# Optimization experiments

Hardware: AMD Instinct MI355X
Metric: run time of the kernel (lower is better)

Reference implementation:

```python
import jax, jax.numpy as jnp
import numpy as np

N, C, L, D, F = 8, 128, 512, 64, 512
ATTN_W = 64
LN_EPS = 1e-5
ATTN_EPS = 1e-6


def _xavier(k, shape):
    lim = float(np.sqrt(6.0 / (shape[0] + shape[1])))
    return jax.random.uniform(k, shape, jnp.float32, -lim, lim)


def setup_inputs() -> dict:
    key = jax.random.key(0)
    ks = jax.random.split(key, 8)
    return dict(
        x=jax.random.normal(ks[0], (N, C, L), jnp.float32),
        Wx=_xavier(ks[1], (C, D)),
        Wt=_xavier(ks[2], (C, D)),
        bh=jnp.zeros((D,), jnp.float32),
        Wa=_xavier(ks[3], (D, 1)),
        ba=jnp.zeros((1,), jnp.float32),
        W0=_xavier(ks[4], (C, F)),
        b0=jnp.zeros((F,), jnp.float32),
        W1=_xavier(ks[5], (F, C)),
        b1=jnp.zeros((C,), jnp.float32),
        g0=jnp.ones((C,), jnp.float32),
        be0=jnp.zeros((C,), jnp.float32),
        g1=jnp.ones((C,), jnp.float32),
        be1=jnp.zeros((C,), jnp.float32),
    )


def _layernorm(y, g, b):
    mu = jnp.mean(y, axis=-1, keepdims=True)
    var = jnp.var(y, axis=-1, keepdims=True)
    return (y - mu) * jax.lax.rsqrt(var + LN_EPS) * g + b


def reference(x, Wx, Wt, bh, Wa, ba, W0, b0, W1, b1, g0, be0, g1, be1):
    xt = jnp.transpose(x, (0, 2, 1))  # (N, L, C)
    q = jnp.einsum('nlc,cd->nld', xt, Wt)  # (N, L, D)
    k = jnp.einsum('nlc,cd->nld', xt, Wx)  # (N, L, D)
    # additive (Bahdanau) scores: h is the large (N, L, L, D) intermediate
    h = jnp.tanh(q[:, :, None, :] + k[:, None, :, :] + bh)
    e = jnp.einsum('nlmd,d->nlm', h, Wa[:, 0]) + ba[0]  # (N, L, L)
    e = jnp.exp(e - jnp.max(e, axis=-1, keepdims=True))
    # local band mask: tril(w//2 - 1) & triu(-w//2) on (row i, col j)
    dij = jnp.arange(L)[None, :] - jnp.arange(L)[:, None]  # j - i
    mask = (dij <= ATTN_W // 2 - 1) & (dij >= -(ATTN_W // 2))
    e = jnp.where(mask, e, 0.0)
    a = e / (jnp.sum(e, axis=-1, keepdims=True) + ATTN_EPS)  # (N, L, L)
    v = jnp.einsum('nlm,nmc->nlc', a, xt)  # (N, L, C)
    x2 = _layernorm(v + xt, g0, be0)
    x3 = jnp.einsum('nlf,fc->nlc', jax.nn.relu(jnp.einsum('nlc,cf->nlf', x2, W0) + b0), W1) + b1
    x4 = _layernorm(x3 + x2, g1, be1)
    return (jnp.transpose(x4, (0, 2, 1)), a)
```

## Files before the change

kernel.cpp:

```cpp
#include <hip/hip_runtime.h>
#include <cstddef>


__global__ __launch_bounds__(256) void prep_kernel(
    const float* __restrict__ x, const float* __restrict__ Wt,
    const float* __restrict__ Wx, float* __restrict__ xt,
    float* __restrict__ q, float* __restrict__ k) {
  __shared__ float xs[128][17];
  int tid = threadIdx.x;
  int bz = blockIdx.x;
  int n = bz >> 6;
  int t6 = bz & 63;
  int l0 = (t6 >> 1) << 4;
  int which = t6 & 1;

  for (int idx = tid; idx < 512; idx += 256) {
    int c = idx >> 2, v = idx & 3;
    float4 d4 = *(const float4*)(x + ((size_t)n * 128 + c) * 512 + l0 + 4 * v);
    xs[c][4 * v + 0] = d4.x; xs[c][4 * v + 1] = d4.y;
    xs[c][4 * v + 2] = d4.z; xs[c][4 * v + 3] = d4.w;
  }
  __syncthreads();

  if (which == 0) {
    for (int idx = tid; idx < 2048; idx += 256) {
      int c = idx & 127, jj = idx >> 7;
      xt[((size_t)n * 512 + l0 + jj) * 128 + c] = xs[c][jj];
    }
  }

  const float* W = which ? Wx : Wt;
  float* dst = which ? k : q;
  int r = tid >> 4;
  int f0 = (tid & 15) << 2;
  float acc[4] = {0.f, 0.f, 0.f, 0.f};
#pragma unroll 4
  for (int cc = 0; cc < 128; cc++) {
    float xv = xs[cc][r];
    float4 w = *(const float4*)(W + cc * 64 + f0);
    acc[0] += xv * w.x; acc[1] += xv * w.y;
    acc[2] += xv * w.z; acc[3] += xv * w.w;
  }
  *(float4*)(dst + ((size_t)n * 512 + l0 + r) * 64 + f0) =
      make_float4(acc[0], acc[1], acc[2], acc[3]);
}

__global__ __launch_bounds__(512, 2) void attn_ffn_fused_kernel(
    const float* __restrict__ q, const float* __restrict__ k,
    const float* __restrict__ bh, const float* __restrict__ Wa,
    const float* __restrict__ ba, const float* __restrict__ xt,
    const float* __restrict__ g0, const float* __restrict__ be0,
    const float* __restrict__ W0, const float* __restrict__ b0,
    const float* __restrict__ W1, const float* __restrict__ b1,
    const float* __restrict__ g1, const float* __restrict__ be1,
    float* __restrict__ a, float* __restrict__ out) {
  __shared__ __align__(16) char smem[81920];
  __shared__ float xst[128][20];
  __shared__ float av[16][64];
  __shared__ float was[64];

  float (*ks)[65] = (float(*)[65])smem;
  float (*qs)[64] = (float(*)[64])(smem + 20544);
  float (*tst)[20] = (float(*)[20])smem;
  float (*part)[16][128] = (float(*)[16][128])(smem + 40960);
  float (*ys)[128] = (float(*)[128])(smem + 73728);

  int tid = threadIdx.x;
  int w = tid >> 6, lane = tid & 63;
  size_t rbase = (size_t)blockIdx.x * 16;
  int n = (int)(rbase >> 9);
  int i0 = (int)(rbase & 511);
  int jlo0 = i0 - 32;

  if (tid < 64) was[tid] = Wa[tid];
  for (int idx = tid; idx < 16 * 16; idx += 512) {
    int r = idx >> 4, d4 = (idx & 15) << 2;
    float4 qv = *(const float4*)(q + ((size_t)n * 512 + i0 + r) * 64 + d4);
    float4 bv = *(const float4*)(bh + d4);
    *(float4*)(&qs[r][d4]) =
        make_float4(qv.x + bv.x, qv.y + bv.y, qv.z + bv.z, qv.w + bv.w);
  }
  for (int idx = tid; idx < 79 * 16; idx += 512) {
    int row = idx >> 4, d4 = (idx & 15) << 2;
    int j = jlo0 + row;
    float4 v = make_float4(0.f, 0.f, 0.f, 0.f);
    if (j >= 0 && j < 512)
      v = *(const float4*)(k + ((size_t)n * 512 + j) * 64 + d4);
    ks[row][d4 + 0] = v.x; ks[row][d4 + 1] = v.y;
    ks[row][d4 + 2] = v.z; ks[row][d4 + 3] = v.w;
  }
  __syncthreads();

#pragma unroll
  for (int rr = 0; rr < 2; rr++) {
    int r = 2 * w + rr;
    int i = i0 + r;
    int j = jlo0 + r + lane;
    bool valid = (j >= 0 && j < 512);
    const float* krow = &ks[r + lane][0];
    float e = 0.f;
#pragma unroll 8
    for (int d = 0; d < 64; d++) {
      float hx = qs[r][d] + krow[d];
      float ex2 = __expf(2.f * hx);
      float th = 1.f - 2.f * __builtin_amdgcn_rcpf(ex2 + 1.f);
      e += was[d] * th;
    }
    e += ba[0];
    if (!valid) e = -1e30f;

    float m = e;
    for (int o = 32; o > 0; o >>= 1) m = fmaxf(m, __shfl_xor(m, o, 64));
    float ex = valid ? __expf(e - m) : 0.f;
    float s = ex;
    for (int o = 32; o > 0; o >>= 1) s += __shfl_xor(s, o, 64);
    av[r][lane] = ex / (s + 1e-6f);

    float* arow = a + ((size_t)n * 512 + i) * 512;
    int jlo = i - 32;
#pragma unroll
    for (int t = 0; t < 2; t++) {
      int col0 = 4 * lane + 256 * t;
      float4 v;
      { int jr = col0 + 0 - jlo; int jc = min(max(jr, 0), 63); v.x = (jr >= 0 && jr < 64) ? av[r][jc] : 0.f; }
      { int jr = col0 + 1 - jlo; int jc = min(max(jr, 0), 63); v.y = (jr >= 0 && jr < 64) ? av[r][jc] : 0.f; }
      { int jr = col0 + 2 - jlo; int jc = min(max(jr, 0), 63); v.z = (jr >= 0 && jr < 64) ? av[r][jc] : 0.f; }
      { int jr = col0 + 3 - jlo; int jc = min(max(jr, 0), 63); v.w = (jr >= 0 && jr < 64) ? av[r][jc] : 0.f; }
      *(float4*)(arow + col0) = v;
    }
  }
  __syncthreads();

  {
    int c = tid & 127;
    int rq = tid >> 7;
    int r0 = rq << 2;
    const float* xtn = xt + (size_t)n * 512 * 128;
    float acc[4] = {0.f, 0.f, 0.f, 0.f};
    int jlo = i0 + r0 - 32;
#pragma unroll
    for (int mm = 0; mm < 67; mm++) {
      int jj = jlo + mm;
      int jc = min(max(jj, 0), 511);
      float xv = xtn[(size_t)jc * 128 + c];
#pragma unroll
      for (int rr = 0; rr < 4; rr++) {
        int mr = mm - rr;
        if (mr >= 0 && mr < 64) acc[rr] += av[r0 + rr][mr] * xv;
      }
    }
#pragma unroll
    for (int rr = 0; rr < 4; rr++) {
      float res = xtn[(size_t)(i0 + r0 + rr) * 128 + c];
      xst[c][r0 + rr] = acc[rr] + res;
    }
  }
  __syncthreads();

#pragma unroll
  for (int rr = 2 * w; rr <= 2 * w + 1; rr++) {
    float a0 = xst[lane][rr], a1 = xst[lane + 64][rr];
    float s = a0 + a1, s2 = a0 * a0 + a1 * a1;
    for (int o = 32; o > 0; o >>= 1) {
      s += __shfl_xor(s, o, 64);
      s2 += __shfl_xor(s2, o, 64);
    }
    float mu = s * (1.f / 128.f);
    float var = s2 * (1.f / 128.f) - mu * mu;
    float rs = rsqrtf(var + 1e-5f);
    xst[lane][rr] = (a0 - mu) * rs * g0[lane] + be0[lane];
    xst[lane + 64][rr] = (a1 - mu) * rs * g0[lane + 64] + be0[lane + 64];
  }
  __syncthreads();

  {
    int fb = tid & 127;
    int r0 = (tid >> 7) << 2;
    float acc[4][4];
#pragma unroll
    for (int i = 0; i < 4; i++)
#pragma unroll
      for (int jj = 0; jj < 4; jj++) acc[i][jj] = 0.f;
#pragma unroll 4
    for (int cc = 0; cc < 128; cc++) {
      float4 xv = *(const float4*)(&xst[cc][r0]);
      float w0 = W0[cc * 512 + fb];
      float w1 = W0[cc * 512 + fb + 128];
      float w2 = W0[cc * 512 + fb + 256];
      float w3 = W0[cc * 512 + fb + 384];
      acc[0][0] += xv.x * w0; acc[1][0] += xv.y * w0; acc[2][0] += xv.z * w0; acc[3][0] += xv.w * w0;
      acc[0][1] += xv.x * w1; acc[1][1] += xv.y * w1; acc[2][1] += xv.z * w1; acc[3][1] += xv.w * w1;
      acc[0][2] += xv.x * w2; acc[1][2] += xv.y * w2; acc[2][2] += xv.z * w2; acc[3][2] += xv.w * w2;
      acc[0][3] += xv.x * w3; acc[1][3] += xv.y * w3; acc[2][3] += xv.z * w3; acc[3][3] += xv.w * w3;
    }
#pragma unroll
    for (int jj = 0; jj < 4; jj++) {
      int f = fb + 128 * jj;
      float bb = b0[f];
      float4 v = make_float4(fmaxf(acc[0][jj] + bb, 0.f), fmaxf(acc[1][jj] + bb, 0.f),
                             fmaxf(acc[2][jj] + bb, 0.f), fmaxf(acc[3][jj] + bb, 0.f));
      *(float4*)(&tst[f][r0]) = v;
    }
  }
  __syncthreads();

  {
    int kq = tid >> 7;
    int c0 = (tid & 31) << 2;
    int r0 = ((tid >> 5) & 3) << 2;
    float acc[4][4];
#pragma unroll
    for (int i = 0; i < 4; i++)
#pragma unroll
      for (int jj = 0; jj < 4; jj++) acc[i][jj] = 0.f;
    const float* W1p = W1 + (size_t)kq * 128 * 128;
    const float(*tstp)[20] = &tst[kq * 128];
#pragma unroll 4
    for (int t = 0; t < 128; t++) {
      float4 wv = *(const float4*)(W1p + t * 128 + c0);
      float4 tv = *(const float4*)(&tstp[t][r0]);
      acc[0][0] += tv.x * wv.x; acc[0][1] += tv.x * wv.y; acc[0][2] += tv.x * wv.z; acc[0][3] += tv.x * wv.w;
      acc[1][0] += tv.y * wv.x; acc[1][1] += tv.y * wv.y; acc[1][2] += tv.y * wv.z; acc[1][3] += tv.y * wv.w;
      acc[2][0] += tv.z * wv.x; acc[2][1] += tv.z * wv.y; acc[2][2] += tv.z * wv.z; acc[2][3] += tv.z * wv.w;
      acc[3][0] += tv.w * wv.x; acc[3][1] += tv.w * wv.y; acc[3][2] += tv.w * wv.z; acc[3][3] += tv.w * wv.w;
    }
#pragma unroll
    for (int i = 0; i < 4; i++) {
      *(float4*)(&part[kq][r0 + i][c0]) =
          make_float4(acc[i][0], acc[i][1], acc[i][2], acc[i][3]);
    }
  }
  __syncthreads();

  for (int idx = tid; idx < 2048; idx += 512) {
    int r = idx >> 7, c = idx & 127;
    ys[r][c] = part[0][r][c] + part[1][r][c] + part[2][r][c] + part[3][r][c] +
               b1[c] + xst[c][r];
  }
  __syncthreads();

#pragma unroll
  for (int rr = 2 * w; rr <= 2 * w + 1; rr++) {
    float a0 = ys[rr][lane], a1 = ys[rr][lane + 64];
    float s = a0 + a1, s2 = a0 * a0 + a1 * a1;
    for (int o = 32; o > 0; o >>= 1) {
      s += __shfl_xor(s, o, 64);
      s2 += __shfl_xor(s2, o, 64);
    }
    float mu = s * (1.f / 128.f);
    float var = s2 * (1.f / 128.f) - mu * mu;
    float rs = rsqrtf(var + 1e-5f);
    ys[rr][lane] = (a0 - mu) * rs * g1[lane] + be1[lane];
    ys[rr][lane + 64] = (a1 - mu) * rs * g1[lane + 64] + be1[lane + 64];
  }
  __syncthreads();

  {
    int c = tid >> 2, tq = tid & 3;
    int l0 = (int)(rbase & 511);
    float4 v = make_float4(ys[4 * tq + 0][c], ys[4 * tq + 1][c],
                           ys[4 * tq + 2][c], ys[4 * tq + 3][c]);
    *(float4*)(out + ((size_t)n * 128 + c) * 512 + l0 + 4 * tq) = v;
  }
}

extern "C" void kernel_launch(void* const* d_in, const int* in_sizes, int n_in,
                              void* d_out, int out_size, void* d_ws, size_t ws_size,
                              hipStream_t stream) {
  const float* x   = (const float*)d_in[0];
  const float* Wx  = (const float*)d_in[1];
  const float* Wt  = (const float*)d_in[2];
  const float* bh  = (const float*)d_in[3];
  const float* Wa  = (const float*)d_in[4];
  const float* ba  = (const float*)d_in[5];
  const float* W0  = (const float*)d_in[6];
  const float* b0  = (const float*)d_in[7];
  const float* W1  = (const float*)d_in[8];
  const float* b1  = (const float*)d_in[9];
  const float* g0  = (const float*)d_in[10];
  const float* be0 = (const float*)d_in[11];
  const float* g1  = (const float*)d_in[12];
  const float* be1 = (const float*)d_in[13];

  float* outx = (float*)d_out;
  float* outa = outx + (size_t)524288;

  float* ws = (float*)d_ws;
  float* xt = ws;
  float* q  = xt + 524288;
  float* k  = q + 262144;

  prep_kernel<<<512, 256, 0, stream>>>(x, Wt, Wx, xt, q, k);
  attn_ffn_fused_kernel<<<256, 512, 0, stream>>>(
      q, k, bh, Wa, ba, xt, g0, be0, W0, b0, W1, b1, g1, be1, outa, outx);
}
```

Before: 132.2 us.

## Halve rows per block to double grid and restructure FFN smem layouts

```diff
diff --git a/kernel.cpp b/kernel.cpp
--- a/kernel.cpp
+++ b/kernel.cpp
@@ -45,7 +45,7 @@
       make_float4(acc[0], acc[1], acc[2], acc[3]);
 }
 
-__global__ __launch_bounds__(512, 2) void attn_ffn_fused_kernel(
+__global__ __launch_bounds__(256, 2) void attn_ffn_fused_kernel(
     const float* __restrict__ q, const float* __restrict__ k,
     const float* __restrict__ bh, const float* __restrict__ Wa,
     const float* __restrict__ ba, const float* __restrict__ xt,
@@ -54,33 +54,33 @@
     const float* __restrict__ W1, const float* __restrict__ b1,
     const float* __restrict__ g1, const float* __restrict__ be1,
     float* __restrict__ a, float* __restrict__ out) {
-  __shared__ __align__(16) char smem[81920];
-  __shared__ float xst[128][20];
-  __shared__ float av[16][64];
+  __shared__ __align__(16) char smem[36992];
+  __shared__ float xst[8][132];
+  __shared__ float av[8][64];
   __shared__ float was[64];
 
   float (*ks)[65] = (float(*)[65])smem;
-  float (*qs)[64] = (float(*)[64])(smem + 20544);
-  float (*tst)[20] = (float(*)[20])smem;
-  float (*part)[16][128] = (float(*)[16][128])(smem + 40960);
-  float (*ys)[128] = (float(*)[128])(smem + 73728);
+  float (*qs)[64] = (float(*)[64])(smem + 18464);
+  float (*tst)[516] = (float(*)[516])smem;
+  float (*part)[8][128] = (float(*)[8][128])(smem + 16512);
+  float (*ys)[128] = (float(*)[128])(smem + 32896);
 
   int tid = threadIdx.x;
   int w = tid >> 6, lane = tid & 63;
-  size_t rbase = (size_t)blockIdx.x * 16;
+  size_t rbase = (size_t)blockIdx.x * 8;
   int n = (int)(rbase >> 9);
   int i0 = (int)(rbase & 511);
   int jlo0 = i0 - 32;
 
   if (tid < 64) was[tid] = Wa[tid];
-  for (int idx = tid; idx < 16 * 16; idx += 512) {
-    int r = idx >> 4, d4 = (idx & 15) << 2;
+  if (tid < 128) {
+    int r = tid >> 4, d4 = (tid & 15) << 2;
     float4 qv = *(const float4*)(q + ((size_t)n * 512 + i0 + r) * 64 + d4);
     float4 bv = *(const float4*)(bh + d4);
     *(float4*)(&qs[r][d4]) =
         make_float4(qv.x + bv.x, qv.y + bv.y, qv.z + bv.z, qv.w + bv.w);
   }
-  for (int idx = tid; idx < 79 * 16; idx += 512) {
+  for (int idx = tid; idx < 71 * 16; idx += 256) {
     int row = idx >> 4, d4 = (idx & 15) << 2;
     int j = jlo0 + row;
     float4 v = make_float4(0.f, 0.f, 0.f, 0.f);
@@ -133,8 +133,7 @@
 
   {
     int c = tid & 127;
-    int rq = tid >> 7;
-    int r0 = rq << 2;
+    int r0 = (tid >> 7) << 2;
     const float* xtn = xt + (size_t)n * 512 * 128;
     float acc[4] = {0.f, 0.f, 0.f, 0.f};
     int jlo = i0 + r0 - 32;
@@ -152,14 +151,14 @@
 #pragma unroll
     for (int rr = 0; rr < 4; rr++) {
       float res = xtn[(size_t)(i0 + r0 + rr) * 128 + c];
-      xst[c][r0 + rr] = acc[rr] + res;
+      xst[r0 + rr][c] = acc[rr] + res;
     }
   }
   __syncthreads();
 
 #pragma unroll
   for (int rr = 2 * w; rr <= 2 * w + 1; rr++) {
-    float a0 = xst[lane][rr], a1 = xst[lane + 64][rr];
+    float a0 = xst[rr][lane], a1 = xst[rr][lane + 64];
     float s = a0 + a1, s2 = a0 * a0 + a1 * a1;
     for (int o = 32; o > 0; o >>= 1) {
       s += __shfl_xor(s, o, 64);
@@ -168,13 +167,13 @@
     float mu = s * (1.f / 128.f);
     float var = s2 * (1.f / 128.f) - mu * mu;
     float rs = rsqrtf(var + 1e-5f);
-    xst[lane][rr] = (a0 - mu) * rs * g0[lane] + be0[lane];
-    xst[lane + 64][rr] = (a1 - mu) * rs * g0[lane + 64] + be0[lane + 64];
+    xst[rr][lane] = (a0 - mu) * rs * g0[lane] + be0[lane];
+    xst[rr][lane + 64] = (a1 - mu) * rs * g0[lane + 64] + be0[lane + 64];
   }
   __syncthreads();
 
   {
-    int fb = tid & 127;
+    int f0 = (tid & 127) << 2;
     int r0 = (tid >> 7) << 2;
     float acc[4][4];
 #pragma unroll
@@ -183,46 +182,51 @@
       for (int jj = 0; jj < 4; jj++) acc[i][jj] = 0.f;
 #pragma unroll 4
     for (int cc = 0; cc < 128; cc++) {
-      float4 xv = *(const float4*)(&xst[cc][r0]);
-      float w0 = W0[cc * 512 + fb];
-      float w1 = W0[cc * 512 + fb + 128];
-      float w2 = W0[cc * 512 + fb + 256];
-      float w3 = W0[cc * 512 + fb + 384];
-      acc[0][0] += xv.x * w0; acc[1][0] += xv.y * w0; acc[2][0] += xv.z * w0; acc[3][0] += xv.w * w0;
-      acc[0][1] += xv.x * w1; acc[1][1] += xv.y * w1; acc[2][1] += xv.z * w1; acc[3][1] += xv.w * w1;
-      acc[0][2] += xv.x * w2; acc[1][2] += xv.y * w2; acc[2][2] += xv.z * w2; acc[3][2] += xv.w * w2;
-      acc[0][3] += xv.x * w3; acc[1][3] += xv.y * w3; acc[2][3] += xv.z * w3; acc[3][3] += xv.w * w3;
-    }
-#pragma unroll
-    for (int jj = 0; jj < 4; jj++) {
-      int f = fb + 128 * jj;
-      float bb = b0[f];
-      float4 v = make_float4(fmaxf(acc[0][jj] + bb, 0.f), fmaxf(acc[1][jj] + bb, 0.f),
-                             fmaxf(acc[2][jj] + bb, 0.f), fmaxf(acc[3][jj] + bb, 0.f));
-      *(float4*)(&tst[f][r0]) = v;
+      float4 wv = *(const float4*)(W0 + cc * 512 + f0);
+      float x0 = xst[r0 + 0][cc];
+      float x1 = xst[r0 + 1][cc];
+      float x2v = xst[r0 + 2][cc];
+      float x3 = xst[r0 + 3][cc];
+      acc[0][0] += x0 * wv.x; acc[0][1] += x0 * wv.y; acc[0][2] += x0 * wv.z; acc[0][3] += x0 * wv.w;
+      acc[1][0] += x1 * wv.x; acc[1][1] += x1 * wv.y; acc[1][2] += x1 * wv.z; acc[1][3] += x1 * wv.w;
+      acc[2][0] += x2v * wv.x; acc[2][1] += x2v * wv.y; acc[2][2] += x2v * wv.z; acc[2][3] += x2v * wv.w;
+      acc[3][0] += x3 * wv.x; acc[3][1] += x3 * wv.y; acc[3][2] += x3 * wv.z; acc[3][3] += x3 * wv.w;
+    }
+    float4 bb = *(const float4*)(b0 + f0);
+#pragma unroll
+    for (int rr = 0; rr < 4; rr++) {
+      float4 v = make_float4(fmaxf(acc[rr][0] + bb.x, 0.f), fmaxf(acc[rr][1] + bb.y, 0.f),
+                             fmaxf(acc[rr][2] + bb.z, 0.f), fmaxf(acc[rr][3] + bb.w, 0.f));
+      *(float4*)(&tst[r0 + rr][f0]) = v;
     }
   }
   __syncthreads();
 
   {
-    int kq = tid >> 7;
-    int c0 = (tid & 31) << 2;
-    int r0 = ((tid >> 5) & 3) << 2;
+    int kq = tid >> 6;
+    int c0 = (lane & 31) << 2;
+    int r0 = (lane >> 5) << 2;
     float acc[4][4];
 #pragma unroll
     for (int i = 0; i < 4; i++)
 #pragma unroll
       for (int jj = 0; jj < 4; jj++) acc[i][jj] = 0.f;
-    const float* W1p = W1 + (size_t)kq * 128 * 128;
-    const float(*tstp)[20] = &tst[kq * 128];
-#pragma unroll 4
-    for (int t = 0; t < 128; t++) {
-      float4 wv = *(const float4*)(W1p + t * 128 + c0);
-      float4 tv = *(const float4*)(&tstp[t][r0]);
-      acc[0][0] += tv.x * wv.x; acc[0][1] += tv.x * wv.y; acc[0][2] += tv.x * wv.z; acc[0][3] += tv.x * wv.w;
-      acc[1][0] += tv.y * wv.x; acc[1][1] += tv.y * wv.y; acc[1][2] += tv.y * wv.z; acc[1][3] += tv.y * wv.w;
-      acc[2][0] += tv.z * wv.x; acc[2][1] += tv.z * wv.y; acc[2][2] += tv.z * wv.z; acc[2][3] += tv.z * wv.w;
-      acc[3][0] += tv.w * wv.x; acc[3][1] += tv.w * wv.y; acc[3][2] += tv.w * wv.z; acc[3][3] += tv.w * wv.w;
+#pragma unroll 2
+    for (int tb = 0; tb < 128; tb += 4) {
+      int tt = kq * 128 + tb;
+      float4 tv0 = *(const float4*)(&tst[r0 + 0][tt]);
+      float4 tv1 = *(const float4*)(&tst[r0 + 1][tt]);
+      float4 tv2 = *(const float4*)(&tst[r0 + 2][tt]);
+      float4 tv3 = *(const float4*)(&tst[r0 + 3][tt]);
+#pragma unroll
+      for (int u = 0; u < 4; u++) {
+        float4 wv = *(const float4*)(W1 + (size_t)(tt + u) * 128 + c0);
+        float t0 = (&tv0.x)[u], t1 = (&tv1.x)[u], t2 = (&tv2.x)[u], t3 = (&tv3.x)[u];
+        acc[0][0] += t0 * wv.x; acc[0][1] += t0 * wv.y; acc[0][2] += t0 * wv.z; acc[0][3] += t0 * wv.w;
+        acc[1][0] += t1 * wv.x; acc[1][1] += t1 * wv.y; acc[1][2] += t1 * wv.z; acc[1][3] += t1 * wv.w;
+        acc[2][0] += t2 * wv.x; acc[2][1] += t2 * wv.y; acc[2][2] += t2 * wv.z; acc[2][3] += t2 * wv.w;
+        acc[3][0] += t3 * wv.x; acc[3][1] += t3 * wv.y; acc[3][2] += t3 * wv.z; acc[3][3] += t3 * wv.w;
+      }
     }
 #pragma unroll
     for (int i = 0; i < 4; i++) {
@@ -232,10 +236,10 @@
   }
   __syncthreads();
 
-  for (int idx = tid; idx < 2048; idx += 512) {
+  for (int idx = tid; idx < 1024; idx += 256) {
     int r = idx >> 7, c = idx & 127;
     ys[r][c] = part[0][r][c] + part[1][r][c] + part[2][r][c] + part[3][r][c] +
-               b1[c] + xst[c][r];
+               b1[c] + xst[r][c];
   }
   __syncthreads();
 
@@ -256,7 +260,7 @@
   __syncthreads();
 
   {
-    int c = tid >> 2, tq = tid & 3;
+    int c = tid >> 1, tq = tid & 1;
     int l0 = (int)(rbase & 511);
     float4 v = make_float4(ys[4 * tq + 0][c], ys[4 * tq + 1][c],
                            ys[4 * tq + 2][c], ys[4 * tq + 3][c]);
@@ -291,6 +295,6 @@
   float* k  = q + 262144;
 
   prep_kernel<<<512, 256, 0, stream>>>(x, Wt, Wx, xt, q, k);
-  attn_ffn_fused_kernel<<<256, 512, 0, stream>>>(
+  attn_ffn_fused_kernel<<<512, 256, 0, stream>>>(
       q, k, bh, Wa, ba, xt, g0, be0, W0, b0, W1, b1, g1, be1, outa, outx);
 }
```

After: 127.1 us. 3.9% less time.

## Halve rows per block and rework fused attention/FFN thread mappings

Applied to the files above, without the earlier changes.

```diff
diff --git a/kernel.cpp b/kernel.cpp
--- a/kernel.cpp
+++ b/kernel.cpp
@@ -45,7 +45,7 @@
       make_float4(acc[0], acc[1], acc[2], acc[3]);
 }
 
-__global__ __launch_bounds__(512, 2) void attn_ffn_fused_kernel(
+__global__ __launch_bounds__(512, 4) void attn_ffn_fused_kernel(
     const float* __restrict__ q, const float* __restrict__ k,
     const float* __restrict__ bh, const float* __restrict__ Wa,
     const float* __restrict__ ba, const float* __restrict__ xt,
@@ -54,57 +54,62 @@
     const float* __restrict__ W1, const float* __restrict__ b1,
     const float* __restrict__ g1, const float* __restrict__ be1,
     float* __restrict__ a, float* __restrict__ out) {
-  __shared__ __align__(16) char smem[81920];
-  __shared__ float xst[128][20];
-  __shared__ float av[16][64];
-  __shared__ float was[64];
-
-  float (*ks)[65] = (float(*)[65])smem;
-  float (*qs)[64] = (float(*)[64])(smem + 20544);
-  float (*tst)[20] = (float(*)[20])smem;
-  float (*part)[16][128] = (float(*)[16][128])(smem + 40960);
-  float (*ys)[128] = (float(*)[128])(smem + 73728);
+  __shared__ __align__(16) char smem[61440];
+  __shared__ __align__(16) float xstT[128][12];
+  __shared__ __align__(16) float avT[71][10];
+  __shared__ __align__(16) float was[64];
+
+  float (*ks)[68] = (float(*)[68])smem;
+  float (*qs)[64] = (float(*)[64])(smem + 19328);
+  float (*tstT)[12] = (float(*)[12])smem;
+  float (*part)[8][128] = (float(*)[8][128])(smem + 24576);
+  float (*ys)[128] = (float(*)[128])(smem + 57344);
 
   int tid = threadIdx.x;
   int w = tid >> 6, lane = tid & 63;
-  size_t rbase = (size_t)blockIdx.x * 16;
+  size_t rbase = (size_t)blockIdx.x * 8;
   int n = (int)(rbase >> 9);
   int i0 = (int)(rbase & 511);
   int jlo0 = i0 - 32;
 
   if (tid < 64) was[tid] = Wa[tid];
-  for (int idx = tid; idx < 16 * 16; idx += 512) {
-    int r = idx >> 4, d4 = (idx & 15) << 2;
+  for (int idx = tid; idx < 71 * 10; idx += 512) ((float*)avT)[idx] = 0.f;
+  if (tid < 128) {
+    int r = tid >> 4, d4 = (tid & 15) << 2;
     float4 qv = *(const float4*)(q + ((size_t)n * 512 + i0 + r) * 64 + d4);
     float4 bv = *(const float4*)(bh + d4);
     *(float4*)(&qs[r][d4]) =
         make_float4(qv.x + bv.x, qv.y + bv.y, qv.z + bv.z, qv.w + bv.w);
   }
-  for (int idx = tid; idx < 79 * 16; idx += 512) {
+  for (int idx = tid; idx < 71 * 16; idx += 512) {
     int row = idx >> 4, d4 = (idx & 15) << 2;
     int j = jlo0 + row;
     float4 v = make_float4(0.f, 0.f, 0.f, 0.f);
     if (j >= 0 && j < 512)
       v = *(const float4*)(k + ((size_t)n * 512 + j) * 64 + d4);
-    ks[row][d4 + 0] = v.x; ks[row][d4 + 1] = v.y;
-    ks[row][d4 + 2] = v.z; ks[row][d4 + 3] = v.w;
-  }
-  __syncthreads();
-
-#pragma unroll
-  for (int rr = 0; rr < 2; rr++) {
-    int r = 2 * w + rr;
+    *(float4*)(&ks[row][d4]) = v;
+  }
+  __syncthreads();
+
+  {
+    int r = w;
     int i = i0 + r;
     int j = jlo0 + r + lane;
     bool valid = (j >= 0 && j < 512);
     const float* krow = &ks[r + lane][0];
     float e = 0.f;
-#pragma unroll 8
-    for (int d = 0; d < 64; d++) {
-      float hx = qs[r][d] + krow[d];
-      float ex2 = __expf(2.f * hx);
-      float th = 1.f - 2.f * __builtin_amdgcn_rcpf(ex2 + 1.f);
-      e += was[d] * th;
+#pragma unroll
+    for (int d4 = 0; d4 < 64; d4 += 4) {
+      float4 kv = *(const float4*)(krow + d4);
+      float4 qv = *(const float4*)(&qs[r][d4]);
+      float4 wv = *(const float4*)(&was[d4]);
+      float h0 = qv.x + kv.x, h1 = qv.y + kv.y;
+      float h2 = qv.z + kv.z, h3 = qv.w + kv.w;
+      float t0 = 1.f - 2.f * __builtin_amdgcn_rcpf(__expf(2.f * h0) + 1.f);
+      float t1 = 1.f - 2.f * __builtin_amdgcn_rcpf(__expf(2.f * h1) + 1.f);
+      float t2 = 1.f - 2.f * __builtin_amdgcn_rcpf(__expf(2.f * h2) + 1.f);
+      float t3 = 1.f - 2.f * __builtin_amdgcn_rcpf(__expf(2.f * h3) + 1.f);
+      e += wv.x * t0 + wv.y * t1 + wv.z * t2 + wv.w * t3;
     }
     e += ba[0];
     if (!valid) e = -1e30f;
@@ -114,7 +119,8 @@
     float ex = valid ? __expf(e - m) : 0.f;
     float s = ex;
     for (int o = 32; o > 0; o >>= 1) s += __shfl_xor(s, o, 64);
-    av[r][lane] = ex / (s + 1e-6f);
+    float aw = ex / (s + 1e-6f);
+    avT[r + lane][r] = aw;
 
     float* arow = a + ((size_t)n * 512 + i) * 512;
     int jlo = i - 32;
@@ -122,10 +128,10 @@
     for (int t = 0; t < 2; t++) {
       int col0 = 4 * lane + 256 * t;
       float4 v;
-      { int jr = col0 + 0 - jlo; int jc = min(max(jr, 0), 63); v.x = (jr >= 0 && jr < 64) ? av[r][jc] : 0.f; }
-      { int jr = col0 + 1 - jlo; int jc = min(max(jr, 0), 63); v.y = (jr >= 0 && jr < 64) ? av[r][jc] : 0.f; }
-      { int jr = col0 + 2 - jlo; int jc = min(max(jr, 0), 63); v.z = (jr >= 0 && jr < 64) ? av[r][jc] : 0.f; }
-      { int jr = col0 + 3 - jlo; int jc = min(max(jr, 0), 63); v.w = (jr >= 0 && jr < 64) ? av[r][jc] : 0.f; }
+      { int jr = col0 + 0 - jlo; int jc = min(max(jr, 0), 63); v.x = (jr >= 0 && jr < 64) ? avT[r + jc][r] : 0.f; }
+      { int jr = col0 + 1 - jlo; int jc = min(max(jr, 0), 63); v.y = (jr >= 0 && jr < 64) ? avT[r + jc][r] : 0.f; }
+      { int jr = col0 + 2 - jlo; int jc = min(max(jr, 0), 63); v.z = (jr >= 0 && jr < 64) ? avT[r + jc][r] : 0.f; }
+      { int jr = col0 + 3 - jlo; int jc = min(max(jr, 0), 63); v.w = (jr >= 0 && jr < 64) ? avT[r + jc][r] : 0.f; }
       *(float4*)(arow + col0) = v;
     }
   }
@@ -133,33 +139,26 @@
 
   {
     int c = tid & 127;
-    int rq = tid >> 7;
-    int r0 = rq << 2;
+    int rh = tid >> 7;
+    int r0 = 2 * rh;
     const float* xtn = xt + (size_t)n * 512 * 128;
-    float acc[4] = {0.f, 0.f, 0.f, 0.f};
-    int jlo = i0 + r0 - 32;
-#pragma unroll
-    for (int mm = 0; mm < 67; mm++) {
-      int jj = jlo + mm;
+    float acc0 = 0.f, acc1 = 0.f;
+    for (int col = r0; col <= r0 + 64; col++) {
+      int jj = jlo0 + col;
       int jc = min(max(jj, 0), 511);
       float xv = xtn[(size_t)jc * 128 + c];
-#pragma unroll
-      for (int rr = 0; rr < 4; rr++) {
-        int mr = mm - rr;
-        if (mr >= 0 && mr < 64) acc[rr] += av[r0 + rr][mr] * xv;
-      }
-    }
-#pragma unroll
-    for (int rr = 0; rr < 4; rr++) {
-      float res = xtn[(size_t)(i0 + r0 + rr) * 128 + c];
-      xst[c][r0 + rr] = acc[rr] + res;
-    }
-  }
-  __syncthreads();
-
-#pragma unroll
-  for (int rr = 2 * w; rr <= 2 * w + 1; rr++) {
-    float a0 = xst[lane][rr], a1 = xst[lane + 64][rr];
+      float2 av2 = *(const float2*)(&avT[col][r0]);
+      acc0 += av2.x * xv;
+      acc1 += av2.y * xv;
+    }
+    float res0 = xtn[(size_t)(i0 + r0) * 128 + c];
+    float res1 = xtn[(size_t)(i0 + r0 + 1) * 128 + c];
+    *(float2*)(&xstT[c][r0]) = make_float2(acc0 + res0, acc1 + res1);
+  }
+  __syncthreads();
+
+  {
+    float a0 = xstT[lane][w], a1 = xstT[lane + 64][w];
     float s = a0 + a1, s2 = a0 * a0 + a1 * a1;
     for (int o = 32; o > 0; o >>= 1) {
       s += __shfl_xor(s, o, 64);
@@ -168,57 +167,72 @@
     float mu = s * (1.f / 128.f);
     float var = s2 * (1.f / 128.f) - mu * mu;
     float rs = rsqrtf(var + 1e-5f);
-    xst[lane][rr] = (a0 - mu) * rs * g0[lane] + be0[lane];
-    xst[lane + 64][rr] = (a1 - mu) * rs * g0[lane + 64] + be0[lane + 64];
-  }
-  __syncthreads();
-
-  {
-    int fb = tid & 127;
-    int r0 = (tid >> 7) << 2;
+    xstT[lane][w] = (a0 - mu) * rs * g0[lane] + be0[lane];
+    xstT[lane + 64][w] = (a1 - mu) * rs * g0[lane + 64] + be0[lane + 64];
+  }
+  __syncthreads();
+
+  {
+    int g = lane & 15;
+    int kq = lane >> 4;
+    int f0 = (16 * w + g) << 2;
+    float acc[8][4];
+#pragma unroll
+    for (int i = 0; i < 8; i++)
+#pragma unroll
+      for (int u = 0; u < 4; u++) acc[i][u] = 0.f;
+    int ccb = kq << 5;
+#pragma unroll 4
+    for (int cc = ccb; cc < ccb + 32; cc++) {
+      float4 xa = *(const float4*)(&xstT[cc][0]);
+      float4 xb = *(const float4*)(&xstT[cc][4]);
+      float4 wv = *(const float4*)(W0 + (size_t)cc * 512 + f0);
+      acc[0][0] += xa.x * wv.x; acc[0][1] += xa.x * wv.y; acc[0][2] += xa.x * wv.z; acc[0][3] += xa.x * wv.w;
+      acc[1][0] += xa.y * wv.x; acc[1][1] += xa.y * wv.y; acc[1][2] += xa.y * wv.z; acc[1][3] += xa.y * wv.w;
+      acc[2][0] += xa.z * wv.x; acc[2][1] += xa.z * wv.y; acc[2][2] += xa.z * wv.z; acc[2][3] += xa.z * wv.w;
+      acc[3][0] += xa.w * wv.x; acc[3][1] += xa.w * wv.y; acc[3][2] += xa.w * wv.z; acc[3][3] += xa.w * wv.w;
+      acc[4][0] += xb.x * wv.x; acc[4][1] += xb.x * wv.y; acc[4][2] += xb.x * wv.z; acc[4][3] += xb.x * wv.w;
+      acc[5][0] += xb.y * wv.x; acc[5][1] += xb.y * wv.y; acc[5][2] += xb.y * wv.z; acc[5][3] += xb.y * wv.w;
+      acc[6][0] += xb.z * wv.x; acc[6][1] += xb.z * wv.y; acc[6][2] += xb.z * wv.z; acc[6][3] += xb.z * wv.w;
+      acc[7][0] += xb.w * wv.x; acc[7][1] += xb.w * wv.y; acc[7][2] += xb.w * wv.z; acc[7][3] += xb.w * wv.w;
+    }
+#pragma unroll
+    for (int i = 0; i < 8; i++)
+#pragma unroll
+      for (int u = 0; u < 4; u++) {
+        float v = acc[i][u];
+        v += __shfl_xor(v, 16, 64);
+        v += __shfl_xor(v, 32, 64);
+        acc[i][u] = v;
+      }
+    int f = f0 + kq;
+    float bb = b0[f];
+    float r0v[8];
+#pragma unroll
+    for (int i = 0; i < 8; i++) {
+      float v = (kq == 0) ? acc[i][0] : (kq == 1) ? acc[i][1]
+              : (kq == 2) ? acc[i][2] : acc[i][3];
+      r0v[i] = fmaxf(v + bb, 0.f);
+    }
+    *(float4*)(&tstT[f][0]) = make_float4(r0v[0], r0v[1], r0v[2], r0v[3]);
+    *(float4*)(&tstT[f][4]) = make_float4(r0v[4], r0v[5], r0v[6], r0v[7]);
+  }
+  __syncthreads();
+
+  {
+    int c0 = (lane & 31) << 2;
+    int rh = lane >> 5;
     float acc[4][4];
 #pragma unroll
     for (int i = 0; i < 4; i++)
 #pragma unroll
-      for (int jj = 0; jj < 4; jj++) acc[i][jj] = 0.f;
+      for (int u = 0; u < 4; u++) acc[i][u] = 0.f;
+    const float* W1p = W1 + (size_t)w * 64 * 128;
+    int tb = w << 6;
 #pragma unroll 4
-    for (int cc = 0; cc < 128; cc++) {
-      float4 xv = *(const float4*)(&xst[cc][r0]);
-      float w0 = W0[cc * 512 + fb];
-      float w1 = W0[cc * 512 + fb + 128];
-      float w2 = W0[cc * 512 + fb + 256];
-      float w3 = W0[cc * 512 + fb + 384];
-      acc[0][0] += xv.x * w0; acc[1][0] += xv.y * w0; acc[2][0] += xv.z * w0; acc[3][0] += xv.w * w0;
-      acc[0][1] += xv.x * w1; acc[1][1] += xv.y * w1; acc[2][1] += xv.z * w1; acc[3][1] += xv.w * w1;
-      acc[0][2] += xv.x * w2; acc[1][2] += xv.y * w2; acc[2][2] += xv.z * w2; acc[3][2] += xv.w * w2;
-      acc[0][3] += xv.x * w3; acc[1][3] += xv.y * w3; acc[2][3] += xv.z * w3; acc[3][3] += xv.w * w3;
-    }
-#pragma unroll
-    for (int jj = 0; jj < 4; jj++) {
-      int f = fb + 128 * jj;
-      float bb = b0[f];
-      float4 v = make_float4(fmaxf(acc[0][jj] + bb, 0.f), fmaxf(acc[1][jj] + bb, 0.f),
-                             fmaxf(acc[2][jj] + bb, 0.f), fmaxf(acc[3][jj] + bb, 0.f));
-      *(float4*)(&tst[f][r0]) = v;
-    }
-  }
-  __syncthreads();
-
-  {
-    int kq = tid >> 7;
-    int c0 = (tid & 31) << 2;
-    int r0 = ((tid >> 5) & 3) << 2;
-    float acc[4][4];
-#pragma unroll
-    for (int i = 0; i < 4; i++)
-#pragma unroll
-      for (int jj = 0; jj < 4; jj++) acc[i][jj] = 0.f;
-    const float* W1p = W1 + (size_t)kq * 128 * 128;
-    const float(*tstp)[20] = &tst[kq * 128];
-#pragma unroll 4
-    for (int t = 0; t < 128; t++) {
-      float4 wv = *(const float4*)(W1p + t * 128 + c0);
-      float4 tv = *(const float4*)(&tstp[t][r0]);
+    for (int t = 0; t < 64; t++) {
+      float4 tv = *(const float4*)(&tstT[tb + t][4 * rh]);
+      float4 wv = *(const float4*)(W1p + (size_t)t * 128 + c0);
       acc[0][0] += tv.x * wv.x; acc[0][1] += tv.x * wv.y; acc[0][2] += tv.x * wv.z; acc[0][3] += tv.x * wv.w;
       acc[1][0] += tv.y * wv.x; acc[1][1] += tv.y * wv.y; acc[1][2] += tv.y * wv.z; acc[1][3] += tv.y * wv.w;
       acc[2][0] += tv.z * wv.x; acc[2][1] += tv.z * wv.y; acc[2][2] += tv.z * wv.z; acc[2][3] += tv.z * wv.w;
@@ -226,22 +240,31 @@
     }
 #pragma unroll
     for (int i = 0; i < 4; i++) {
-      *(float4*)(&part[kq][r0 + i][c0]) =
+      *(float4*)(&part[w][4 * rh + i][c0]) =
           make_float4(acc[i][0], acc[i][1], acc[i][2], acc[i][3]);
     }
   }
   __syncthreads();
 
-  for (int idx = tid; idx < 2048; idx += 512) {
-    int r = idx >> 7, c = idx & 127;
-    ys[r][c] = part[0][r][c] + part[1][r][c] + part[2][r][c] + part[3][r][c] +
-               b1[c] + xst[c][r];
-  }
-  __syncthreads();
-
-#pragma unroll
-  for (int rr = 2 * w; rr <= 2 * w + 1; rr++) {
-    float a0 = ys[rr][lane], a1 = ys[rr][lane + 64];
+  if (tid < 256) {
+    int r = tid >> 5, c0 = (tid & 31) << 2;
+    float4 s = make_float4(0.f, 0.f, 0.f, 0.f);
+#pragma unroll
+    for (int ko = 0; ko < 8; ko++) {
+      float4 p = *(const float4*)(&part[ko][r][c0]);
+      s.x += p.x; s.y += p.y; s.z += p.z; s.w += p.w;
+    }
+    float4 bv = *(const float4*)(b1 + c0);
+    s.x += bv.x + xstT[c0 + 0][r];
+    s.y += bv.y + xstT[c0 + 1][r];
+    s.z += bv.z + xstT[c0 + 2][r];
+    s.w += bv.w + xstT[c0 + 3][r];
+    *(float4*)(&ys[r][c0]) = s;
+  }
+  __syncthreads();
+
+  {
+    float a0 = ys[w][lane], a1 = ys[w][lane + 64];
     float s = a0 + a1, s2 = a0 * a0 + a1 * a1;
     for (int o = 32; o > 0; o >>= 1) {
       s += __shfl_xor(s, o, 64);
@@ -250,17 +273,15 @@
     float mu = s * (1.f / 128.f);
     float var = s2 * (1.f / 128.f) - mu * mu;
     float rs = rsqrtf(var + 1e-5f);
-    ys[rr][lane] = (a0 - mu) * rs * g1[lane] + be1[lane];
-    ys[rr][lane + 64] = (a1 - mu) * rs * g1[lane + 64] + be1[lane + 64];
+    ys[w][lane] = (a0 - mu) * rs * g1[lane] + be1[lane];
+    ys[w][lane + 64] = (a1 - mu) * rs * g1[lane + 64] + be1[lane + 64];
   }
   __syncthreads();
 
   {
     int c = tid >> 2, tq = tid & 3;
-    int l0 = (int)(rbase & 511);
-    float4 v = make_float4(ys[4 * tq + 0][c], ys[4 * tq + 1][c],
-                           ys[4 * tq + 2][c], ys[4 * tq + 3][c]);
-    *(float4*)(out + ((size_t)n * 128 + c) * 512 + l0 + 4 * tq) = v;
+    *(float2*)(out + ((size_t)n * 128 + c) * 512 + i0 + 2 * tq) =
+        make_float2(ys[2 * tq][c], ys[2 * tq + 1][c]);
   }
 }
 
@@ -291,6 +312,6 @@
   float* k  = q + 262144;
 
   prep_kernel<<<512, 256, 0, stream>>>(x, Wt, Wx, xt, q, k);
-  attn_ffn_fused_kernel<<<256, 512, 0, stream>>>(
+  attn_ffn_fused_kernel<<<512, 512, 0, stream>>>(
       q, k, bh, Wa, ba, xt, g0, be0, W0, b0, W1, b1, g1, be1, outa, outx);
 }
```

New measurement: 124.9 us. 1.06x faster.
